# Optimization experiments

Hardware: AMD Instinct MI355X
Metric: run time of the kernel (lower is better)

## Reference

```python
import jax, jax.numpy as jnp
import numpy as np

B, N, H, E, STEPS = 16, 512, 128, 4, 5
ANNO = 1


def _edge_states(y):
    # y: [B, N, H*E] -> torch view(B,N,H,E).transpose(2,3).transpose(1,2) -> [B,E,N,H] -> [B,N*E,H]
    return y.reshape(B, N, H, E).transpose(0, 3, 1, 2).reshape(B, N * E, H)


def setup_inputs() -> dict:
    key = jax.random.key(0)
    ks = jax.random.split(key, 20)
    s = 0.05
    inp = {
        "x": jax.random.normal(ks[0], (B, N, H), jnp.float32),
        "a": jax.random.normal(ks[1], (B, N, ANNO), jnp.float32),
        "m": jax.random.uniform(ks[2], (B, N, N * E * 2), jnp.float32),
        # fc_in / fc_out: Linear(H, H*E); weights stored [in, out]
        "W_in": jax.random.normal(ks[3], (H, H * E), jnp.float32) * s,
        "b_in": jnp.zeros((H * E,), jnp.float32),
        "W_out": jax.random.normal(ks[4], (H, H * E), jnp.float32) * s,
        "b_out": jnp.zeros((H * E,), jnp.float32),
        # GatedPropagation gates: Linear(3H, H)
        "W_z": jax.random.normal(ks[5], (3 * H, H), jnp.float32) * s,
        "b_z": jnp.zeros((H,), jnp.float32),
        "W_r": jax.random.normal(ks[6], (3 * H, H), jnp.float32) * s,
        "b_r": jnp.zeros((H,), jnp.float32),
        "W_t": jax.random.normal(ks[7], (3 * H, H), jnp.float32) * s,
        "b_t": jnp.zeros((H,), jnp.float32),
        # output head: fc1(H+ANNO, H), fc2(H, 1)
        "W1": jax.random.normal(ks[8], (H + ANNO, H), jnp.float32) * s,
        "b1": jnp.zeros((H,), jnp.float32),
        "W2": jax.random.normal(ks[9], (H, 1), jnp.float32) * s,
        "b2": jnp.zeros((1,), jnp.float32),
    }
    return inp


def reference(x, a, m, W_in, b_in, W_out, b_out, W_z, b_z, W_r, b_r, W_t, b_t, W1, b1, W2, b2):
    m_in = m[:, :, : N * E]   # [B, N, N*E]
    m_out = m[:, :, N * E :]  # [B, N, N*E]
    h = x
    for _ in range(STEPS):
        in_states = _edge_states(h @ W_in + b_in)    # [B, N*E, H]
        out_states = _edge_states(h @ W_out + b_out)  # [B, N*E, H]
        a_in = jnp.einsum('bnm,bmh->bnh', m_in, in_states)
        a_out = jnp.einsum('bnm,bmh->bnh', m_out, out_states)
        cat = jnp.concatenate((a_in, a_out, h), axis=2)  # [B, N, 3H]
        z = jax.nn.sigmoid(cat @ W_z + b_z)
        r = jax.nn.sigmoid(cat @ W_r + b_r)
        joint = jnp.concatenate((a_in, a_out, r * h), axis=2)
        h_hat = jnp.tanh(joint @ W_t + b_t)
        h = (1 - z) * h + z * h_hat
    feat = jnp.tanh(jnp.concatenate((h, a), axis=2) @ W1 + b1)  # [B, N, H]
    out = (feat @ W2 + b2).sum(axis=2)  # [B, N]
    return out
```

## Files before the change

### kernel.cpp

```cpp
#include <hip/hip_runtime.h>
#include <math.h>

#define BB 16
#define NN 512
#define HH 128
#define EE 4
#define NSTEPS 5
#define ROWS (BB*NN)
#define KDIM (NN*EE)

typedef _Float16 f16x8 __attribute__((ext_vector_type(8)));
typedef float f32x4 __attribute__((ext_vector_type(4)));

#define MFMA(a,b,c) __builtin_amdgcn_mfma_f32_16x16x32_f16(a, b, c, 0, 0, 0)

__device__ inline void split8v(float4 u, float4 v, f16x8& hi, f16x8& lo) {
    float f[8] = {u.x, u.y, u.z, u.w, v.x, v.y, v.z, v.w};
    #pragma unroll
    for (int i = 0; i < 8; i++) {
        _Float16 h = (_Float16)f[i];
        hi[i] = h;
        lo[i] = (_Float16)(f[i] - (float)h);
    }
}

__device__ inline void split1(float v, _Float16* __restrict__ hp, _Float16* __restrict__ lp) {
    _Float16 h = (_Float16)v;
    *hp = h;
    *lp = (_Float16)(v - (float)h);
}

__device__ __forceinline__ void async16(void* lds, const void* g) {
    __builtin_amdgcn_global_load_lds(
        (const __attribute__((address_space(1))) void*)g,
        (__attribute__((address_space(3))) void*)lds,
        16, 0, 0);
}

__global__ void prep_kernel(const float* __restrict__ x,
                            const float* __restrict__ W_in, const float* __restrict__ b_in,
                            const float* __restrict__ W_out, const float* __restrict__ b_out,
                            const float* __restrict__ W_z, const float* __restrict__ W_r,
                            const float* __restrict__ W_t, const float* __restrict__ W1,
                            _Float16* __restrict__ WpTh, _Float16* __restrict__ WpTl,
                            float* __restrict__ bp,
                            _Float16* __restrict__ WzrtH, _Float16* __restrict__ WzrtL,
                            _Float16* __restrict__ Wt1h, _Float16* __restrict__ Wt1l,
                            _Float16* __restrict__ hHi, _Float16* __restrict__ hLo,
                            _Float16* __restrict__ W1Th, _Float16* __restrict__ W1Tl) {
    int idx = blockIdx.x * 256 + threadIdx.x;
    if (idx < 131072) {
        int c = idx >> 7, k = idx & 127;
        int io = c >> 9, cc = c & 511, e = cc >> 7, hh = cc & 127;
        const float* W = io ? W_out : W_in;
        split1(W[k * 512 + hh * 4 + e], WpTh + idx, WpTl + idx);
        if (k == 0) bp[c] = (io ? b_out : b_in)[hh * 4 + e];
    } else if (idx < 131072 + 147456) {
        int j = idx - 131072;
        int c = j / 384, k = j - c * 384;
        float v;
        if (c < 128)      v = W_z[k * 128 + c];
        else if (c < 256) v = W_r[k * 128 + (c - 128)];
        else              v = (k < 256) ? W_t[k * 128 + (c - 256)] : 0.0f;
        split1(v, WzrtH + j, WzrtL + j);
    } else if (idx < 131072 + 147456 + 16384) {
        int j = idx - 131072 - 147456;
        int c = j >> 7, k = j & 127;
        split1(W_t[(256 + k) * 128 + c], Wt1h + j, Wt1l + j);
    } else if (idx < 131072 + 147456 + 16384 + 1048576) {
        int j = idx - 131072 - 147456 - 16384;
        split1(x[j], hHi + j, hLo + j);
    } else if (idx < 131072 + 147456 + 16384 + 1048576 + 16384) {
        int j = idx - (131072 + 147456 + 16384 + 1048576);
        int c = j >> 7, k = j & 127;
        split1(W1[k * 128 + c], W1Th + j, W1Tl + j);
    }
}

__global__ __launch_bounds__(256) void xw_mfma(
        const _Float16* __restrict__ hHi, const _Float16* __restrict__ hLo,
        const _Float16* __restrict__ WpTh, const _Float16* __restrict__ WpTl,
        const float* __restrict__ bp,
        _Float16* __restrict__ YpTh, _Float16* __restrict__ YpTl) {
    const int tid = threadIdx.x;
    const int c0 = blockIdx.x * 64;
    const int n0 = blockIdx.y * 128;
    const int b  = blockIdx.z;
    const int w = tid >> 6, l = tid & 63;
    const int lm = l & 15, q = l >> 4;
    const int wr = (w & 1) * 32, wc = (w >> 1) * 64;
    f32x4 zero = {0.f, 0.f, 0.f, 0.f};
    f32x4 acc[2][4];
    #pragma unroll
    for (int i = 0; i < 2; i++)
        #pragma unroll
        for (int j = 0; j < 4; j++) acc[i][j] = zero;
    const size_t aoff = (size_t)(c0 + wr + lm) * 128 + q * 8;
    const size_t boff = (size_t)(b * 512 + n0 + wc + lm) * 128 + q * 8;
    #pragma unroll
    for (int ki = 0; ki < 4; ki++) {
        const int kc = ki * 32;
        f16x8 a0h = *(const f16x8*)(WpTh + aoff + kc);
        f16x8 a0l = *(const f16x8*)(WpTl + aoff + kc);
        f16x8 a1h = *(const f16x8*)(WpTh + aoff + 16 * 128 + kc);
        f16x8 a1l = *(const f16x8*)(WpTl + aoff + 16 * 128 + kc);
        #pragma unroll
        for (int ct = 0; ct < 4; ct++) {
            f16x8 bh = *(const f16x8*)(hHi + boff + (size_t)(ct * 16) * 128 + kc);
            f16x8 bl = *(const f16x8*)(hLo + boff + (size_t)(ct * 16) * 128 + kc);
            acc[0][ct] = MFMA(a0h, bh, acc[0][ct]);
            acc[0][ct] = MFMA(a0h, bl, acc[0][ct]);
            acc[0][ct] = MFMA(a0l, bh, acc[0][ct]);
            acc[1][ct] = MFMA(a1h, bh, acc[1][ct]);
            acc[1][ct] = MFMA(a1h, bl, acc[1][ct]);
            acc[1][ct] = MFMA(a1l, bh, acc[1][ct]);
        }
    }
    #pragma unroll
    for (int rg = 0; rg < 2; rg++)
        #pragma unroll
        for (int rr = 0; rr < 4; rr++) {
            int c = c0 + wr + rg * 16 + q * 4 + rr;
            float bias = bp[c];
            size_t d = ((size_t)b * 1024 + c) * 512 + n0 + wc + lm;
            #pragma unroll
            for (int ct = 0; ct < 4; ct++) {
                float v = acc[rg][ct][rr] + bias;
                split1(v, YpTh + d + ct * 16, YpTl + d + ct * 16);
            }
        }
}

__global__ __launch_bounds__(512, 4) void msg_mfma(const float* __restrict__ m,
        const _Float16* __restrict__ YpTh, const _Float16* __restrict__ YpTl,
        float* __restrict__ Apart) {
    __shared__ float    mlds[2][128 * 32];
    __shared__ _Float16 ylds[2][128 * 64];

    const int tid = threadIdx.x;
    const int w = tid >> 6, l = tid & 63;
    const int lm = l & 15, q = l >> 4;
    const int wr = (w & 3) * 32;
    const int wc = (w >> 2) * 64;

    const int wg = blockIdx.x;
    const int xcd = wg & 7;
    const int s8  = wg >> 3;
    const int gi  = s8 >> 2;
    const int t4  = s8 & 3;
    const int g   = gi * 8 + xcd;
    const int kz  = g & 3;
    const int biz = g >> 2;
    const int b = biz >> 1, io = biz & 1;
    const int n0 = t4 * 128;

    const float*    mg  = m    + (size_t)(b * 512 + n0) * 4096 + io * 2048 + kz * 512;
    const _Float16* yhg = YpTh + (size_t)(b * 1024 + io * 512 + kz * 128) * 512;
    const _Float16* ylg = YpTl + (size_t)(b * 1024 + io * 512 + kz * 128) * 512;

    f32x4 zero = {0.f, 0.f, 0.f, 0.f};
    f32x4 acc[2][4];
    #pragma unroll
    for (int i = 0; i < 2; i++)
        #pragma unroll
        for (int j = 0; j < 4; j++) acc[i][j] = zero;

    #define STAGE(buf, kt) do {                                                \
        _Pragma("unroll")                                                      \
        for (int j = 0; j < 2; j++) {                  \
            int gi2 = (w * 2 + j) * 64 + l;                                    \
            int r = gi2 >> 3, pg = gi2 & 7;                                    \
            int lg = pg ^ (r & 7);                                             \
            async16(&mlds[buf][(w * 2 + j) * 256],                             \
                    mg + (size_t)r * 4096 + (size_t)(kt) * 32 + lg * 4);       \
        }                                                                      \
        _Pragma("unroll")                                                      \
        for (int j = 0; j < 2; j++) {          \
            int gi2 = (w * 2 + j) * 64 + l;                                    \
            int r = gi2 >> 3, pg = gi2 & 7;                                    \
            int lg = pg ^ (r & 7);                                             \
            const _Float16* src = (lg < 4 ? yhg : ylg)                         \
                + (size_t)r * 512 + (size_t)(kt) * 32 + (lg & 3) * 8;          \
            async16(&ylds[buf][(w * 2 + j) * 512], src);                       \
        }                                                                      \
    } while (0)

    #define COMPUTE(buf) do {                                                  \
        f16x8 ah[2], al[2];                                                    \
        _Pragma("unroll")                                                      \
        for (int rg = 0; rg < 2; rg++) {                                       \
            int r = wr + rg * 16 + lm, sw = r & 7;                             \
            const float* mrow = &mlds[buf][r * 32];                            \
            float4 u = *(const float4*)(mrow + (((2 * q) ^ sw) * 4));          \
            float4 v = *(const float4*)(mrow + (((2 * q + 1) ^ sw) * 4));      \
            split8v(u, v, ah[rg], al[rg]);                                     \
        }                                                                      \
        _Pragma("unroll")                                                      \
        for (int ct = 0; ct < 4; ct++) {                                       \
            int r = wc + ct * 16 + lm, sw = r & 7;                             \
            const _Float16* yrow = &ylds[buf][r * 64];                         \
            f16x8 bh = *(const f16x8*)(yrow + ((q ^ sw) * 8));                 \
            f16x8 bl = *(const f16x8*)(yrow + (((4 + q) ^ sw) * 8));           \
            acc[0][ct] = MFMA(ah[0], bh, acc[0][ct]);                          \
            acc[0][ct] = MFMA(ah[0], bl, acc[0][ct]);                          \
            acc[0][ct] = MFMA(al[0], bh, acc[0][ct]);                          \
            acc[1][ct] = MFMA(ah[1], bh, acc[1][ct]);                          \
            acc[1][ct] = MFMA(ah[1], bl, acc[1][ct]);                          \
            acc[1][ct] = MFMA(al[1], bh, acc[1][ct]);                          \
        }                                                                      \
    } while (0)

    STAGE(0, 0);
    #pragma unroll
    for (int t = 0; t < 16; t++) {
        if (t < 15) {
            STAGE((t + 1) & 1, t + 1);
            asm volatile("s_waitcnt vmcnt(4)" ::: "memory");
        } else {
            asm volatile("s_waitcnt vmcnt(0)" ::: "memory");
        }
        __builtin_amdgcn_s_barrier();
        __builtin_amdgcn_sched_barrier(0);
        COMPUTE(t & 1);
        __builtin_amdgcn_s_barrier();
    }
    #undef STAGE
    #undef COMPUTE

    float* Ap = Apart + (((size_t)(kz * 32 + biz) * 512) + n0 + wr) * 128 + wc;
    #pragma unroll
    for (int rg = 0; rg < 2; rg++)
        #pragma unroll
        for (int ct = 0; ct < 4; ct++)
            #pragma unroll
            for (int rr = 0; rr < 4; rr++)
                Ap[(size_t)(rg * 16 + q * 4 + rr) * 128 + ct * 16 + lm] = acc[rg][ct][rr];
}

__global__ __launch_bounds__(256) void msg_reduce(const float* __restrict__ Apart,
        _Float16* __restrict__ AinH, _Float16* __restrict__ AinL,
        _Float16* __restrict__ AoutH, _Float16* __restrict__ AoutL) {
    const size_t SL = (size_t)32 * 512 * 128;
    size_t idx = ((size_t)blockIdx.x * 256 + threadIdx.x) * 4;
    float4 v0 = *(const float4*)(Apart + idx);
    float4 v1 = *(const float4*)(Apart + idx + SL);
    float4 v2 = *(const float4*)(Apart + idx + 2 * SL);
    float4 v3 = *(const float4*)(Apart + idx + 3 * SL);
    float s[4] = {v0.x + v1.x + v2.x + v3.x, v0.y + v1.y + v2.y + v3.y,
                  v0.z + v1.z + v2.z + v3.z, v0.w + v1.w + v2.w + v3.w};
    int biz = (int)(idx >> 16);
    int rem = (int)(idx & 65535);
    int b = biz >> 1, io = biz & 1;
    size_t d = ((size_t)b << 16) + rem;
    _Float16* Ah = (io ? AoutH : AinH) + d;
    _Float16* Al = (io ? AoutL : AinL) + d;
    #pragma unroll
    for (int j = 0; j < 4; j++) split1(s[j], Ah + j, Al + j);
}

__global__ __launch_bounds__(256) void gate_gemm1(
        const _Float16* __restrict__ AinH, const _Float16* __restrict__ AinL,
        const _Float16* __restrict__ AoutH, const _Float16* __restrict__ AoutL,
        const _Float16* __restrict__ hHi, const _Float16* __restrict__ hLo,
        const _Float16* __restrict__ WzrtH, const _Float16* __restrict__ WzrtL,
        const float* __restrict__ hcur, const float* __restrict__ b_r,
        float* __restrict__ ZRT,
        _Float16* __restrict__ RHh, _Float16* __restrict__ RHl) {
    const int tid = threadIdx.x;
    const int row0 = blockIdx.x * 64;
    const int c0 = blockIdx.y * 128;
    const int w = tid >> 6, l = tid & 63;
    const int lm = l & 15, q = l >> 4;
    const int wr = (w & 1) * 32, wc = (w >> 1) * 64;
    const size_t rA0 = (size_t)(row0 + wr + lm) * 128 + q * 8;
    const size_t rA1 = rA0 + 16 * 128;
    f32x4 zero = {0.f, 0.f, 0.f, 0.f};
    f32x4 acc[2][4];
    #pragma unroll
    for (int i = 0; i < 2; i++)
        #pragma unroll
        for (int j = 0; j < 4; j++) acc[i][j] = zero;
    const size_t woff = (size_t)(c0 + wc + lm) * 384 + q * 8;
    #pragma unroll
    for (int ph = 0; ph < 3; ph++) {
        const _Float16* Xh = (ph == 0) ? AinH : (ph == 1) ? AoutH : hHi;
        const _Float16* Xl = (ph == 0) ? AinL : (ph == 1) ? AoutL : hLo;
        #pragma unroll
        for (int ki = 0; ki < 4; ki++) {
            const int kc = ki * 32;
            f16x8 a0h = *(const f16x8*)(Xh + rA0 + kc);
            f16x8 a0l = *(const f16x8*)(Xl + rA0 + kc);
            f16x8 a1h = *(const f16x8*)(Xh + rA1 + kc);
            f16x8 a1l = *(const f16x8*)(Xl + rA1 + kc);
            const int kg = ph * 128 + kc;
            #pragma unroll
            for (int ct = 0; ct < 4; ct++) {
                f16x8 bh = *(const f16x8*)(WzrtH + woff + (size_t)(ct * 16) * 384 + kg);
                f16x8 bl = *(const f16x8*)(WzrtL + woff + (size_t)(ct * 16) * 384 + kg);
                acc[0][ct] = MFMA(a0h, bh, acc[0][ct]);
                acc[0][ct] = MFMA(a0h, bl, acc[0][ct]);
                acc[0][ct] = MFMA(a0l, bh, acc[0][ct]);
                acc[1][ct] = MFMA(a1h, bh, acc[1][ct]);
                acc[1][ct] = MFMA(a1h, bl, acc[1][ct]);
                acc[1][ct] = MFMA(a1l, bh, acc[1][ct]);
            }
        }
    }
    if (blockIdx.y == 1) {
        #pragma unroll
        for (int rg = 0; rg < 2; rg++)
            #pragma unroll
            for (int ct = 0; ct < 4; ct++)
                #pragma unroll
                for (int rr = 0; rr < 4; rr++) {
                    int grow = row0 + wr + rg * 16 + q * 4 + rr;
                    int col = wc + ct * 16 + lm;
                    float rp = acc[rg][ct][rr] + b_r[col];
                    float r = 1.0f / (1.0f + expf(-rp));
                    size_t d = (size_t)grow * 128 + col;
                    split1(r * hcur[d], RHh + d, RHl + d);
                }
    } else {
        #pragma unroll
        for (int rg = 0; rg < 2; rg++)
            #pragma unroll
            for (int ct = 0; ct < 4; ct++)
                #pragma unroll
                for (int rr = 0; rr < 4; rr++)
                    ZRT[(size_t)(row0 + wr + rg * 16 + q * 4 + rr) * 384 + c0 + wc + ct * 16 + lm] =
                        acc[rg][ct][rr];
    }
}

__global__ __launch_bounds__(256) void gate_gemm2(
        const _Float16* __restrict__ RHh, const _Float16* __restrict__ RHl,
        const _Float16* __restrict__ Wt1h, const _Float16* __restrict__ Wt1l,
        const float* __restrict__ ZRT, const float* __restrict__ hcur,
        const float* __restrict__ b_z, const float* __restrict__ b_t,
        float* __restrict__ hnF, _Float16* __restrict__ hnH, _Float16* __restrict__ hnL) {
    const int tid = threadIdx.x;
    const int row0 = blockIdx.x * 32;
    const int w = tid >> 6, l = tid & 63;
    const int lm = l & 15, q = l >> 4;
    const int wr = (w & 1) * 16, wc = (w >> 1) * 64;
    f32x4 zero = {0.f, 0.f, 0.f, 0.f};
    f32x4 acc[4] = {zero, zero, zero, zero};
    const size_t aoff = (size_t)(row0 + wr + lm) * 128 + q * 8;
    const size_t woff = (size_t)(wc + lm) * 128 + q * 8;
    #pragma unroll
    for (int ki = 0; ki < 4; ki++) {
        const int kc = ki * 32;
        f16x8 ah = *(const f16x8*)(RHh + aoff + kc);
        f16x8 al = *(const f16x8*)(RHl + aoff + kc);
        #pragma unroll
        for (int ct = 0; ct < 4; ct++) {
            f16x8 bh = *(const f16x8*)(Wt1h + woff + (size_t)(ct * 16) * 128 + kc);
            f16x8 bl = *(const f16x8*)(Wt1l + woff + (size_t)(ct * 16) * 128 + kc);
            acc[ct] = MFMA(ah, bh, acc[ct]);
            acc[ct] = MFMA(ah, bl, acc[ct]);
            acc[ct] = MFMA(al, bh, acc[ct]);
        }
    }
    #pragma unroll
    for (int ct = 0; ct < 4; ct++)
        #pragma unroll
        for (int rr = 0; rr < 4; rr++) {
            int grow = row0 + wr + q * 4 + rr;
            int col = wc + ct * 16 + lm;
            float tp = acc[ct][rr] + ZRT[(size_t)grow * 384 + 256 + col] + b_t[col];
            float hhat = tanhf(tp);
            float zp = ZRT[(size_t)grow * 384 + col] + b_z[col];
            float z = 1.0f / (1.0f + expf(-zp));
            float hv = hcur[(size_t)grow * 128 + col];
            float hn = (1.0f - z) * hv + z * hhat;
            size_t d = (size_t)grow * 128 + col;
            hnF[d] = hn;
            split1(hn, hnH + d, hnL + d);
        }
}

__global__ __launch_bounds__(256) void out_mfma(
        const _Float16* __restrict__ hH, const _Float16* __restrict__ hL,
        const _Float16* __restrict__ W1Th, const _Float16* __restrict__ W1Tl,
        const float* __restrict__ W1, const float* __restrict__ a,
        const float* __restrict__ b1, const float* __restrict__ W2,
        const float* __restrict__ b2, float* __restrict__ out) {
    __shared__ float red[4][16];
    const int tid = threadIdx.x;
    const int row0 = blockIdx.x * 32;
    const int w = tid >> 6, l = tid & 63;
    const int lm = l & 15, q = l >> 4;
    const int wr = (w & 1) * 16, wc = (w >> 1) * 64;
    f32x4 zero = {0.f, 0.f, 0.f, 0.f};
    f32x4 acc[4] = {zero, zero, zero, zero};
    const size_t aoff = (size_t)(row0 + wr + lm) * 128 + q * 8;
    const size_t woff = (size_t)(wc + lm) * 128 + q * 8;
    #pragma unroll
    for (int ki = 0; ki < 4; ki++) {
        const int kc = ki * 32;
        f16x8 ah = *(const f16x8*)(hH + aoff + kc);
        f16x8 al = *(const f16x8*)(hL + aoff + kc);
        #pragma unroll
        for (int ct = 0; ct < 4; ct++) {
            f16x8 bh = *(const f16x8*)(W1Th + woff + (size_t)(ct * 16) * 128 + kc);
            f16x8 bl = *(const f16x8*)(W1Tl + woff + (size_t)(ct * 16) * 128 + kc);
            acc[ct] = MFMA(ah, bh, acc[ct]);
            acc[ct] = MFMA(ah, bl, acc[ct]);
            acc[ct] = MFMA(al, bh, acc[ct]);
        }
    }
    float psum[4] = {0.f, 0.f, 0.f, 0.f};
    #pragma unroll
    for (int ct = 0; ct < 4; ct++) {
        int col = wc + ct * 16 + lm;
        float w2v = W2[col];
        float w1last = W1[128 * 128 + col];
        float b1v = b1[col];
        #pragma unroll
        for (int rr = 0; rr < 4; rr++) {
            int grow = row0 + wr + q * 4 + rr;
            float pre = acc[ct][rr] + a[grow] * w1last + b1v;
            psum[rr] += tanhf(pre) * w2v;
        }
    }
    #pragma unroll
    for (int rr = 0; rr < 4; rr++) {
        float p = psum[rr];
        p += __shfl_xor(p, 1, 64);
        p += __shfl_xor(p, 2, 64);
        p += __shfl_xor(p, 4, 64);
        p += __shfl_xor(p, 8, 64);
        if (lm == 0) red[w][q * 4 + rr] = p;
    }
    __syncthreads();
    if (tid < 32) {
        int r = tid;
        int wsel = (r >> 4) & 1;
        out[row0 + r] = red[wsel][r & 15] + red[wsel + 2][r & 15] + b2[0];
    }
}

extern "C" void kernel_launch(void* const* d_in, const int* in_sizes, int n_in,
                              void* d_out, int out_size, void* d_ws, size_t ws_size,
                              hipStream_t stream) {
    const float* x    = (const float*)d_in[0];
    const float* a    = (const float*)d_in[1];
    const float* m    = (const float*)d_in[2];
    const float* W_in = (const float*)d_in[3];
    const float* b_in = (const float*)d_in[4];
    const float* W_out= (const float*)d_in[5];
    const float* b_out= (const float*)d_in[6];
    const float* W_z  = (const float*)d_in[7];
    const float* b_z  = (const float*)d_in[8];
    const float* W_r  = (const float*)d_in[9];
    const float* b_r  = (const float*)d_in[10];
    const float* W_t  = (const float*)d_in[11];
    const float* b_t  = (const float*)d_in[12];
    const float* W1   = (const float*)d_in[13];
    const float* b1   = (const float*)d_in[14];
    const float* W2   = (const float*)d_in[15];
    const float* b2   = (const float*)d_in[16];
    float* out = (float*)d_out;

    char* p = (char*)d_ws;
    _Float16* WpTh  = (_Float16*)p; p += 262144;
    _Float16* WpTl  = (_Float16*)p; p += 262144;
    float*    bp    = (float*)p;    p += 4096;
    _Float16* WzrtH = (_Float16*)p; p += 294912;
    _Float16* WzrtL = (_Float16*)p; p += 294912;
    _Float16* Wt1h  = (_Float16*)p; p += 32768;
    _Float16* Wt1l  = (_Float16*)p; p += 32768;
    _Float16* W1Th  = (_Float16*)p; p += 32768;
    _Float16* W1Tl  = (_Float16*)p; p += 32768;
    _Float16* YpTh  = (_Float16*)p; p += 16777216;
    _Float16* YpTl  = (_Float16*)p; p += 16777216;
    _Float16* AinH  = (_Float16*)p; p += 2097152;
    _Float16* AinL  = (_Float16*)p; p += 2097152;
    _Float16* AoutH = (_Float16*)p; p += 2097152;
    _Float16* AoutL = (_Float16*)p; p += 2097152;
    _Float16* RHh   = (_Float16*)p; p += 2097152;
    _Float16* RHl   = (_Float16*)p; p += 2097152;
    float*    ZRT   = (float*)p;    p += 12582912;
    float*    hA    = (float*)p;    p += 4194304;
    float*    hB    = (float*)p;    p += 4194304;
    _Float16* hHiA  = (_Float16*)p; p += 2097152;
    _Float16* hLoA  = (_Float16*)p; p += 2097152;
    _Float16* hHiB  = (_Float16*)p; p += 2097152;
    _Float16* hLoB  = (_Float16*)p; p += 2097152;
    float*    Apart = (float*)p;    p += 33554432;

    prep_kernel<<<5312, 256, 0, stream>>>(x, W_in, b_in, W_out, b_out, W_z, W_r, W_t,
                                          W1, WpTh, WpTl, bp, WzrtH, WzrtL, Wt1h, Wt1l,
                                          hHiA, hLoA, W1Th, W1Tl);

    const float* curF = x;
    const _Float16 *curH = hHiA, *curL = hLoA;
    for (int s = 0; s < NSTEPS; s++) {
        float*    nF = (s & 1) ? hB : hA;
        _Float16* nH = (s & 1) ? hHiA : hHiB;
        _Float16* nL = (s & 1) ? hLoA : hLoB;
        xw_mfma<<<dim3(16, 4, 16), 256, 0, stream>>>(curH, curL, WpTh, WpTl, bp, YpTh, YpTl);
        msg_mfma<<<dim3(512), 512, 0, stream>>>(m, YpTh, YpTl, Apart);
        msg_reduce<<<2048, 256, 0, stream>>>(Apart, AinH, AinL, AoutH, AoutL);
        gate_gemm1<<<dim3(128, 3), 256, 0, stream>>>(AinH, AinL, AoutH, AoutL,
                                                     curH, curL, WzrtH, WzrtL,
                                                     curF, b_r, ZRT, RHh, RHl);
        gate_gemm2<<<256, 256, 0, stream>>>(RHh, RHl, Wt1h, Wt1l, ZRT, curF,
                                            b_z, b_t, nF, nH, nL);
        curF = nF; curH = nH; curL = nL;
    }
    out_mfma<<<256, 256, 0, stream>>>(curH, curL, W1Th, W1Tl, W1, a, b1, W2, b2, out);
}
```

Baseline: 787.0 us.

## Halve split-K in message GEMM and fuse partial reduction into gate GEMM

```diff
diff --git a/kernel.cpp b/kernel.cpp
--- a/kernel.cpp
+++ b/kernel.cpp
@@ -28,6 +28,10 @@
     _Float16 h = (_Float16)v;
     *hp = h;
     *lp = (_Float16)(v - (float)h);
+}
+
+__device__ inline float4 f4add(float4 a, float4 b) {
+    return make_float4(a.x + b.x, a.y + b.y, a.z + b.z, a.w + b.w);
 }
 
 __device__ __forceinline__ void async16(void* lds, const void* g) {
@@ -145,18 +149,16 @@
 
     const int wg = blockIdx.x;
     const int xcd = wg & 7;
-    const int s8  = wg >> 3;
-    const int gi  = s8 >> 2;
-    const int t4  = s8 & 3;
+    const int t4  = (wg >> 3) & 3;
+    const int gi  = wg >> 5;
     const int g   = gi * 8 + xcd;
-    const int kz  = g & 3;
-    const int biz = g >> 2;
+    const int ez  = g & 1, biz = g >> 1;
     const int b = biz >> 1, io = biz & 1;
     const int n0 = t4 * 128;
 
-    const float*    mg  = m    + (size_t)(b * 512 + n0) * 4096 + io * 2048 + kz * 512;
-    const _Float16* yhg = YpTh + (size_t)(b * 1024 + io * 512 + kz * 128) * 512;
-    const _Float16* ylg = YpTl + (size_t)(b * 1024 + io * 512 + kz * 128) * 512;
+    const float*    mg  = m    + (size_t)(b * 512 + n0) * 4096 + io * 2048 + ez * 1024;
+    const _Float16* yhg = YpTh + (size_t)(b * 1024 + io * 512 + ez * 256) * 512;
+    const _Float16* ylg = YpTl + (size_t)(b * 1024 + io * 512 + ez * 256) * 512;
 
     f32x4 zero = {0.f, 0.f, 0.f, 0.f};
     f32x4 acc[2][4];
@@ -165,14 +167,16 @@
         #pragma unroll
         for (int j = 0; j < 4; j++) acc[i][j] = zero;
 
-    #define STAGE(buf, kt) do {                                                \
+    #define STAGE(buf, eee, kt) do {                                           \
+        const size_t moff = (size_t)(eee) * 512 + (size_t)(kt) * 32;           \
+        const size_t yoff = (size_t)(eee) * 65536 + (size_t)(kt) * 32;         \
         _Pragma("unroll")                                                      \
         for (int j = 0; j < 2; j++) {                  \
             int gi2 = (w * 2 + j) * 64 + l;                                    \
             int r = gi2 >> 3, pg = gi2 & 7;                                    \
             int lg = pg ^ (r & 7);                                             \
             async16(&mlds[buf][(w * 2 + j) * 256],                             \
-                    mg + (size_t)r * 4096 + (size_t)(kt) * 32 + lg * 4);       \
+                    mg + (size_t)r * 4096 + moff + lg * 4);                    \
         }                                                                      \
         _Pragma("unroll")                                                      \
         for (int j = 0; j < 2; j++) {          \
@@ -180,7 +184,7 @@
             int r = gi2 >> 3, pg = gi2 & 7;                                    \
             int lg = pg ^ (r & 7);                                             \
             const _Float16* src = (lg < 4 ? yhg : ylg)                         \
-                + (size_t)r * 512 + (size_t)(kt) * 32 + (lg & 3) * 8;          \
+                + (size_t)r * 512 + yoff + (lg & 3) * 8;                       \
             async16(&ylds[buf][(w * 2 + j) * 512], src);                       \
         }                                                                      \
     } while (0)
@@ -210,11 +214,12 @@
         }                                                                      \
     } while (0)
 
-    STAGE(0, 0);
-    #pragma unroll
-    for (int t = 0; t < 16; t++) {
-        if (t < 15) {
-            STAGE((t + 1) & 1, t + 1);
+    STAGE(0, 0, 0);
+    #pragma unroll
+    for (int t = 0; t < 32; t++) {
+        if (t < 31) {
+            const int t2 = t + 1;
+            STAGE(t2 & 1, t2 >> 4, t2 & 15);
             asm volatile("s_waitcnt vmcnt(4)" ::: "memory");
         } else {
             asm volatile("s_waitcnt vmcnt(0)" ::: "memory");
@@ -227,7 +232,7 @@
     #undef STAGE
     #undef COMPUTE
 
-    float* Ap = Apart + (((size_t)(kz * 32 + biz) * 512) + n0 + wr) * 128 + wc;
+    float* Ap = Apart + (((size_t)(ez * 32 + biz) * 512) + n0 + wr) * 128 + wc;
     #pragma unroll
     for (int rg = 0; rg < 2; rg++)
         #pragma unroll
@@ -237,35 +242,14 @@
                 Ap[(size_t)(rg * 16 + q * 4 + rr) * 128 + ct * 16 + lm] = acc[rg][ct][rr];
 }
 
-__global__ __launch_bounds__(256) void msg_reduce(const float* __restrict__ Apart,
-        _Float16* __restrict__ AinH, _Float16* __restrict__ AinL,
-        _Float16* __restrict__ AoutH, _Float16* __restrict__ AoutL) {
-    const size_t SL = (size_t)32 * 512 * 128;
-    size_t idx = ((size_t)blockIdx.x * 256 + threadIdx.x) * 4;
-    float4 v0 = *(const float4*)(Apart + idx);
-    float4 v1 = *(const float4*)(Apart + idx + SL);
-    float4 v2 = *(const float4*)(Apart + idx + 2 * SL);
-    float4 v3 = *(const float4*)(Apart + idx + 3 * SL);
-    float s[4] = {v0.x + v1.x + v2.x + v3.x, v0.y + v1.y + v2.y + v3.y,
-                  v0.z + v1.z + v2.z + v3.z, v0.w + v1.w + v2.w + v3.w};
-    int biz = (int)(idx >> 16);
-    int rem = (int)(idx & 65535);
-    int b = biz >> 1, io = biz & 1;
-    size_t d = ((size_t)b << 16) + rem;
-    _Float16* Ah = (io ? AoutH : AinH) + d;
-    _Float16* Al = (io ? AoutL : AinL) + d;
-    #pragma unroll
-    for (int j = 0; j < 4; j++) split1(s[j], Ah + j, Al + j);
-}
-
 __global__ __launch_bounds__(256) void gate_gemm1(
-        const _Float16* __restrict__ AinH, const _Float16* __restrict__ AinL,
-        const _Float16* __restrict__ AoutH, const _Float16* __restrict__ AoutL,
+        const float* __restrict__ Apart,
         const _Float16* __restrict__ hHi, const _Float16* __restrict__ hLo,
         const _Float16* __restrict__ WzrtH, const _Float16* __restrict__ WzrtL,
         const float* __restrict__ hcur, const float* __restrict__ b_r,
         float* __restrict__ ZRT,
         _Float16* __restrict__ RHh, _Float16* __restrict__ RHl) {
+    const size_t SL2 = (size_t)32 * 512 * 128;
     const int tid = threadIdx.x;
     const int row0 = blockIdx.x * 64;
     const int c0 = blockIdx.y * 128;
@@ -274,6 +258,8 @@
     const int wr = (w & 1) * 32, wc = (w >> 1) * 64;
     const size_t rA0 = (size_t)(row0 + wr + lm) * 128 + q * 8;
     const size_t rA1 = rA0 + 16 * 128;
+    const int bb2 = (row0 >> 9) * 2;
+    const int nn  = (row0 & 511) + wr + lm;
     f32x4 zero = {0.f, 0.f, 0.f, 0.f};
     f32x4 acc[2][4];
     #pragma unroll
@@ -283,15 +269,25 @@
     const size_t woff = (size_t)(c0 + wc + lm) * 384 + q * 8;
     #pragma unroll
     for (int ph = 0; ph < 3; ph++) {
-        const _Float16* Xh = (ph == 0) ? AinH : (ph == 1) ? AoutH : hHi;
-        const _Float16* Xl = (ph == 0) ? AinL : (ph == 1) ? AoutL : hLo;
         #pragma unroll
         for (int ki = 0; ki < 4; ki++) {
             const int kc = ki * 32;
-            f16x8 a0h = *(const f16x8*)(Xh + rA0 + kc);
-            f16x8 a0l = *(const f16x8*)(Xl + rA0 + kc);
-            f16x8 a1h = *(const f16x8*)(Xh + rA1 + kc);
-            f16x8 a1l = *(const f16x8*)(Xl + rA1 + kc);
+            f16x8 a0h, a0l, a1h, a1l;
+            if (ph < 2) {
+                const float* A = Apart + ((size_t)(bb2 + ph) * 512 + nn) * 128 + q * 8 + kc;
+                float4 u0 = f4add(*(const float4*)A,       *(const float4*)(A + SL2));
+                float4 u1 = f4add(*(const float4*)(A + 4), *(const float4*)(A + SL2 + 4));
+                split8v(u0, u1, a0h, a0l);
+                const float* B = A + 16 * 128;
+                float4 v0 = f4add(*(const float4*)B,       *(const float4*)(B + SL2));
+                float4 v1 = f4add(*(const float4*)(B + 4), *(const float4*)(B + SL2 + 4));
+                split8v(v0, v1, a1h, a1l);
+            } else {
+                a0h = *(const f16x8*)(hHi + rA0 + kc);
+                a0l = *(const f16x8*)(hLo + rA0 + kc);
+                a1h = *(const f16x8*)(hHi + rA1 + kc);
+                a1l = *(const f16x8*)(hLo + rA1 + kc);
+            }
             const int kg = ph * 128 + kc;
             #pragma unroll
             for (int ct = 0; ct < 4; ct++) {
@@ -474,10 +470,6 @@
     _Float16* W1Tl  = (_Float16*)p; p += 32768;
     _Float16* YpTh  = (_Float16*)p; p += 16777216;
     _Float16* YpTl  = (_Float16*)p; p += 16777216;
-    _Float16* AinH  = (_Float16*)p; p += 2097152;
-    _Float16* AinL  = (_Float16*)p; p += 2097152;
-    _Float16* AoutH = (_Float16*)p; p += 2097152;
-    _Float16* AoutL = (_Float16*)p; p += 2097152;
     _Float16* RHh   = (_Float16*)p; p += 2097152;
     _Float16* RHl   = (_Float16*)p; p += 2097152;
     float*    ZRT   = (float*)p;    p += 12582912;
@@ -487,7 +479,7 @@
     _Float16* hLoA  = (_Float16*)p; p += 2097152;
     _Float16* hHiB  = (_Float16*)p; p += 2097152;
     _Float16* hLoB  = (_Float16*)p; p += 2097152;
-    float*    Apart = (float*)p;    p += 33554432;
+    float*    Apart = (float*)p;    p += 16777216;
 
     prep_kernel<<<5312, 256, 0, stream>>>(x, W_in, b_in, W_out, b_out, W_z, W_r, W_t,
                                           W1, WpTh, WpTl, bp, WzrtH, WzrtL, Wt1h, Wt1l,
@@ -500,10 +492,8 @@
         _Float16* nH = (s & 1) ? hHiA : hHiB;
         _Float16* nL = (s & 1) ? hLoA : hLoB;
         xw_mfma<<<dim3(16, 4, 16), 256, 0, stream>>>(curH, curL, WpTh, WpTl, bp, YpTh, YpTl);
-        msg_mfma<<<dim3(512), 512, 0, stream>>>(m, YpTh, YpTl, Apart);
-        msg_reduce<<<2048, 256, 0, stream>>>(Apart, AinH, AinL, AoutH, AoutL);
-        gate_gemm1<<<dim3(128, 3), 256, 0, stream>>>(AinH, AinL, AoutH, AoutL,
-                                                     curH, curL, WzrtH, WzrtL,
+        msg_mfma<<<dim3(256), 512, 0, stream>>>(m, YpTh, YpTl, Apart);
+        gate_gemm1<<<dim3(128, 3), 256, 0, stream>>>(Apart, curH, curL, WzrtH, WzrtL,
                                                      curF, b_r, ZRT, RHh, RHl);
         gate_gemm2<<<256, 256, 0, stream>>>(RHh, RHl, Wt1h, Wt1l, ZRT, curF,
                                             b_z, b_t, nF, nH, nL);
```

Result: slower. 829.1 us (+5.3%).

## Fuse gate GEMMs into one kernel with z/r/t pre-activations in shared memory

Applied to the files above, without the earlier changes.

```diff
diff --git a/kernel.cpp b/kernel.cpp
--- a/kernel.cpp
+++ b/kernel.cpp
@@ -258,125 +258,115 @@
     for (int j = 0; j < 4; j++) split1(s[j], Ah + j, Al + j);
 }
 
-__global__ __launch_bounds__(256) void gate_gemm1(
+__global__ __launch_bounds__(256) void gate_fused(
         const _Float16* __restrict__ AinH, const _Float16* __restrict__ AinL,
         const _Float16* __restrict__ AoutH, const _Float16* __restrict__ AoutL,
         const _Float16* __restrict__ hHi, const _Float16* __restrict__ hLo,
         const _Float16* __restrict__ WzrtH, const _Float16* __restrict__ WzrtL,
-        const float* __restrict__ hcur, const float* __restrict__ b_r,
-        float* __restrict__ ZRT,
-        _Float16* __restrict__ RHh, _Float16* __restrict__ RHl) {
-    const int tid = threadIdx.x;
-    const int row0 = blockIdx.x * 64;
-    const int c0 = blockIdx.y * 128;
-    const int w = tid >> 6, l = tid & 63;
-    const int lm = l & 15, q = l >> 4;
-    const int wr = (w & 1) * 32, wc = (w >> 1) * 64;
-    const size_t rA0 = (size_t)(row0 + wr + lm) * 128 + q * 8;
-    const size_t rA1 = rA0 + 16 * 128;
-    f32x4 zero = {0.f, 0.f, 0.f, 0.f};
-    f32x4 acc[2][4];
-    #pragma unroll
-    for (int i = 0; i < 2; i++)
-        #pragma unroll
-        for (int j = 0; j < 4; j++) acc[i][j] = zero;
-    const size_t woff = (size_t)(c0 + wc + lm) * 384 + q * 8;
-    #pragma unroll
-    for (int ph = 0; ph < 3; ph++) {
-        const _Float16* Xh = (ph == 0) ? AinH : (ph == 1) ? AoutH : hHi;
-        const _Float16* Xl = (ph == 0) ? AinL : (ph == 1) ? AoutL : hLo;
-        #pragma unroll
-        for (int ki = 0; ki < 4; ki++) {
-            const int kc = ki * 32;
-            f16x8 a0h = *(const f16x8*)(Xh + rA0 + kc);
-            f16x8 a0l = *(const f16x8*)(Xl + rA0 + kc);
-            f16x8 a1h = *(const f16x8*)(Xh + rA1 + kc);
-            f16x8 a1l = *(const f16x8*)(Xl + rA1 + kc);
-            const int kg = ph * 128 + kc;
-            #pragma unroll
-            for (int ct = 0; ct < 4; ct++) {
-                f16x8 bh = *(const f16x8*)(WzrtH + woff + (size_t)(ct * 16) * 384 + kg);
-                f16x8 bl = *(const f16x8*)(WzrtL + woff + (size_t)(ct * 16) * 384 + kg);
-                acc[0][ct] = MFMA(a0h, bh, acc[0][ct]);
-                acc[0][ct] = MFMA(a0h, bl, acc[0][ct]);
-                acc[0][ct] = MFMA(a0l, bh, acc[0][ct]);
-                acc[1][ct] = MFMA(a1h, bh, acc[1][ct]);
-                acc[1][ct] = MFMA(a1h, bl, acc[1][ct]);
-                acc[1][ct] = MFMA(a1l, bh, acc[1][ct]);
-            }
-        }
-    }
-    if (blockIdx.y == 1) {
-        #pragma unroll
-        for (int rg = 0; rg < 2; rg++)
-            #pragma unroll
-            for (int ct = 0; ct < 4; ct++)
-                #pragma unroll
-                for (int rr = 0; rr < 4; rr++) {
-                    int grow = row0 + wr + rg * 16 + q * 4 + rr;
-                    int col = wc + ct * 16 + lm;
-                    float rp = acc[rg][ct][rr] + b_r[col];
-                    float r = 1.0f / (1.0f + expf(-rp));
-                    size_t d = (size_t)grow * 128 + col;
-                    split1(r * hcur[d], RHh + d, RHl + d);
-                }
-    } else {
-        #pragma unroll
-        for (int rg = 0; rg < 2; rg++)
-            #pragma unroll
-            for (int ct = 0; ct < 4; ct++)
-                #pragma unroll
-                for (int rr = 0; rr < 4; rr++)
-                    ZRT[(size_t)(row0 + wr + rg * 16 + q * 4 + rr) * 384 + c0 + wc + ct * 16 + lm] =
-                        acc[rg][ct][rr];
-    }
-}
-
-__global__ __launch_bounds__(256) void gate_gemm2(
-        const _Float16* __restrict__ RHh, const _Float16* __restrict__ RHl,
         const _Float16* __restrict__ Wt1h, const _Float16* __restrict__ Wt1l,
-        const float* __restrict__ ZRT, const float* __restrict__ hcur,
-        const float* __restrict__ b_z, const float* __restrict__ b_t,
+        const float* __restrict__ hcur,
+        const float* __restrict__ b_z, const float* __restrict__ b_r,
+        const float* __restrict__ b_t,
         float* __restrict__ hnF, _Float16* __restrict__ hnH, _Float16* __restrict__ hnL) {
+    __shared__ float zrt[32][388];
     const int tid = threadIdx.x;
     const int row0 = blockIdx.x * 32;
     const int w = tid >> 6, l = tid & 63;
     const int lm = l & 15, q = l >> 4;
-    const int wr = (w & 1) * 16, wc = (w >> 1) * 64;
     f32x4 zero = {0.f, 0.f, 0.f, 0.f};
-    f32x4 acc[4] = {zero, zero, zero, zero};
-    const size_t aoff = (size_t)(row0 + wr + lm) * 128 + q * 8;
-    const size_t woff = (size_t)(wc + lm) * 128 + q * 8;
-    #pragma unroll
-    for (int ki = 0; ki < 4; ki++) {
-        const int kc = ki * 32;
-        f16x8 ah = *(const f16x8*)(RHh + aoff + kc);
-        f16x8 al = *(const f16x8*)(RHl + aoff + kc);
-        #pragma unroll
-        for (int ct = 0; ct < 4; ct++) {
-            f16x8 bh = *(const f16x8*)(Wt1h + woff + (size_t)(ct * 16) * 128 + kc);
-            f16x8 bl = *(const f16x8*)(Wt1l + woff + (size_t)(ct * 16) * 128 + kc);
-            acc[ct] = MFMA(ah, bh, acc[ct]);
-            acc[ct] = MFMA(ah, bl, acc[ct]);
-            acc[ct] = MFMA(al, bh, acc[ct]);
-        }
-    }
-    #pragma unroll
-    for (int ct = 0; ct < 4; ct++)
-        #pragma unroll
-        for (int rr = 0; rr < 4; rr++) {
-            int grow = row0 + wr + q * 4 + rr;
-            int col = wc + ct * 16 + lm;
-            float tp = acc[ct][rr] + ZRT[(size_t)grow * 384 + 256 + col] + b_t[col];
-            float hhat = tanhf(tp);
-            float zp = ZRT[(size_t)grow * 384 + col] + b_z[col];
-            float z = 1.0f / (1.0f + expf(-zp));
-            float hv = hcur[(size_t)grow * 128 + col];
-            float hn = (1.0f - z) * hv + z * hhat;
-            size_t d = (size_t)grow * 128 + col;
-            hnF[d] = hn;
-            split1(hn, hnH + d, hnL + d);
-        }
+
+    {
+        const int wc1 = w * 96;
+        f32x4 acc[2][6];
+        #pragma unroll
+        for (int i = 0; i < 2; i++)
+            #pragma unroll
+            for (int j = 0; j < 6; j++) acc[i][j] = zero;
+        const size_t rA0 = (size_t)(row0 + lm) * 128 + q * 8;
+        const size_t rA1 = rA0 + 16 * 128;
+        const size_t woff = (size_t)(wc1 + lm) * 384 + q * 8;
+        #pragma unroll
+        for (int ph = 0; ph < 3; ph++) {
+            const _Float16* Xh = (ph == 0) ? AinH : (ph == 1) ? AoutH : hHi;
+            const _Float16* Xl = (ph == 0) ? AinL : (ph == 1) ? AoutL : hLo;
+            #pragma unroll
+            for (int ki = 0; ki < 4; ki++) {
+                const int kc = ki * 32;
+                f16x8 a0h = *(const f16x8*)(Xh + rA0 + kc);
+                f16x8 a0l = *(const f16x8*)(Xl + rA0 + kc);
+                f16x8 a1h = *(const f16x8*)(Xh + rA1 + kc);
+                f16x8 a1l = *(const f16x8*)(Xl + rA1 + kc);
+                const int kg = ph * 128 + kc;
+                #pragma unroll
+                for (int ct = 0; ct < 6; ct++) {
+                    f16x8 bh = *(const f16x8*)(WzrtH + woff + (size_t)(ct * 16) * 384 + kg);
+                    f16x8 bl = *(const f16x8*)(WzrtL + woff + (size_t)(ct * 16) * 384 + kg);
+                    acc[0][ct] = MFMA(a0h, bh, acc[0][ct]);
+                    acc[0][ct] = MFMA(a0h, bl, acc[0][ct]);
+                    acc[0][ct] = MFMA(a0l, bh, acc[0][ct]);
+                    acc[1][ct] = MFMA(a1h, bh, acc[1][ct]);
+                    acc[1][ct] = MFMA(a1h, bl, acc[1][ct]);
+                    acc[1][ct] = MFMA(a1l, bh, acc[1][ct]);
+                }
+            }
+        }
+        #pragma unroll
+        for (int rg = 0; rg < 2; rg++)
+            #pragma unroll
+            for (int ct = 0; ct < 6; ct++)
+                #pragma unroll
+                for (int rr = 0; rr < 4; rr++)
+                    zrt[rg * 16 + q * 4 + rr][wc1 + ct * 16 + lm] = acc[rg][ct][rr];
+    }
+    __syncthreads();
+
+    {
+        const int wr2 = (w & 1) * 16, wc2 = (w >> 1) * 64;
+        f32x4 acc2[4] = {zero, zero, zero, zero};
+        const int arow = wr2 + lm;
+        const size_t woff2 = (size_t)(wc2 + lm) * 128 + q * 8;
+        #pragma unroll
+        for (int ki = 0; ki < 4; ki++) {
+            const int kc = ki * 32;
+            const int k0 = kc + q * 8;
+            float rh[8];
+            #pragma unroll
+            for (int j = 0; j < 8; j++) {
+                int k = k0 + j;
+                float rp = zrt[arow][128 + k] + b_r[k];
+                float r = 1.0f / (1.0f + expf(-rp));
+                rh[j] = r * hcur[(size_t)(row0 + arow) * 128 + k];
+            }
+            float4 u = make_float4(rh[0], rh[1], rh[2], rh[3]);
+            float4 v = make_float4(rh[4], rh[5], rh[6], rh[7]);
+            f16x8 ah, al;
+            split8v(u, v, ah, al);
+            #pragma unroll
+            for (int ct = 0; ct < 4; ct++) {
+                f16x8 bh = *(const f16x8*)(Wt1h + woff2 + (size_t)(ct * 16) * 128 + kc);
+                f16x8 bl = *(const f16x8*)(Wt1l + woff2 + (size_t)(ct * 16) * 128 + kc);
+                acc2[ct] = MFMA(ah, bh, acc2[ct]);
+                acc2[ct] = MFMA(ah, bl, acc2[ct]);
+                acc2[ct] = MFMA(al, bh, acc2[ct]);
+            }
+        }
+        #pragma unroll
+        for (int ct = 0; ct < 4; ct++)
+            #pragma unroll
+            for (int rr = 0; rr < 4; rr++) {
+                int lrow = wr2 + q * 4 + rr;
+                int col = wc2 + ct * 16 + lm;
+                float tp = acc2[ct][rr] + zrt[lrow][256 + col] + b_t[col];
+                float hhat = tanhf(tp);
+                float zp = zrt[lrow][col] + b_z[col];
+                float z = 1.0f / (1.0f + expf(-zp));
+                size_t d = (size_t)(row0 + lrow) * 128 + col;
+                float hv = hcur[d];
+                float hn = (1.0f - z) * hv + z * hhat;
+                hnF[d] = hn;
+                split1(hn, hnH + d, hnL + d);
+            }
+    }
 }
 
 __global__ __launch_bounds__(256) void out_mfma(
@@ -478,9 +468,6 @@
     _Float16* AinL  = (_Float16*)p; p += 2097152;
     _Float16* AoutH = (_Float16*)p; p += 2097152;
     _Float16* AoutL = (_Float16*)p; p += 2097152;
-    _Float16* RHh   = (_Float16*)p; p += 2097152;
-    _Float16* RHl   = (_Float16*)p; p += 2097152;
-    float*    ZRT   = (float*)p;    p += 12582912;
     float*    hA    = (float*)p;    p += 4194304;
     float*    hB    = (float*)p;    p += 4194304;
     _Float16* hHiA  = (_Float16*)p; p += 2097152;
@@ -502,11 +489,9 @@
         xw_mfma<<<dim3(16, 4, 16), 256, 0, stream>>>(curH, curL, WpTh, WpTl, bp, YpTh, YpTl);
         msg_mfma<<<dim3(512), 512, 0, stream>>>(m, YpTh, YpTl, Apart);
         msg_reduce<<<2048, 256, 0, stream>>>(Apart, AinH, AinL, AoutH, AoutL);
-        gate_gemm1<<<dim3(128, 3), 256, 0, stream>>>(AinH, AinL, AoutH, AoutL,
-                                                     curH, curL, WzrtH, WzrtL,
-                                                     curF, b_r, ZRT, RHh, RHl);
-        gate_gemm2<<<256, 256, 0, stream>>>(RHh, RHl, Wt1h, Wt1l, ZRT, curF,
-                                            b_z, b_t, nF, nH, nL);
+        gate_fused<<<256, 256, 0, stream>>>(AinH, AinL, AoutH, AoutL, curH, curL,
+                                            WzrtH, WzrtL, Wt1h, Wt1l, curF,
+                                            b_z, b_r, b_t, nF, nH, nL);
         curF = nF; curH = nH; curL = nL;
     }
     out_mfma<<<256, 256, 0, stream>>>(curH, curL, W1Th, W1Tl, W1, a, b1, W2, b2, out);
```

New measurement: 755.9 us. -4.0%, faster.
